# Optimization experiments

Measured on AMD Instinct MI355X. Metric: run time of the kernel, lower is better.

## Reference

```python
import jax, jax.numpy as jnp
import numpy as np

L, T, F = 16, 1 << 19, 2
N_MIN, N_MAX = 16, 2048
N_POINTS = 1 << 21
_PRIMES = (np.uint32(1), np.uint32(2654435761))


def _resolutions(L, N_min, N_max):
    if L == 1:
        return [N_min]
    b = (N_max / N_min) ** (1.0 / (L - 1))
    return [int(round(N_min * b ** l)) for l in range(L)]


def _hash(cx, cy, table_size):
    # XOR of coord_i * prime_i, mod T. T is a power of two, so uint32
    # wraparound matches torch's int64 arithmetic in the low bits.
    h = cx.astype(jnp.uint32) * _PRIMES[0]
    h = h ^ (cy.astype(jnp.uint32) * _PRIMES[1])
    return (h % jnp.uint32(table_size)).astype(jnp.int32)


def setup_inputs() -> dict:
    key = jax.random.key(0)
    k1, k2 = jax.random.split(key)
    xy = jax.random.uniform(k1, (N_POINTS, 2), dtype=jnp.float32)
    # matches torch.empty(T,F).uniform_(-1e-4, 1e-4) per level
    tables = (jax.random.uniform(k2, (L, T, F), dtype=jnp.float32) * 2.0 - 1.0) * 1e-4
    return {"xy": xy, "tables": tables}


def reference(xy, tables):
    # xy: (P, 2) in [0,1]; tables: (L, T, F). Returns (P, L*F).
    res = _resolutions(L, N_MIN, N_MAX)
    feats = []
    for l in range(L):
        N = res[l]
        scaled = xy * N                      # (P, 2)
        i0 = jnp.floor(scaled).astype(jnp.int32)
        t = scaled - i0.astype(xy.dtype)
        wx, wy = t[..., 0:1], t[..., 1:2]    # (P, 1)
        corners = []
        for dy in (0, 1):
            for dx in (0, 1):
                cx = (i0[..., 0] + dx) % N
                cy = (i0[..., 1] + dy) % N
                h = _hash(cx, cy, T)         # (P,)
                corners.append(tables[l][h]) # (P, F)
        c00, c10, c01, c11 = corners
        f0 = c00 * (1 - wx) + c10 * wx
        f1 = c01 * (1 - wx) + c11 * wx
        feats.append(f0 * (1 - wy) + f1 * wy)
    return jnp.concatenate(feats, axis=-1)   # (P, L*F)
```

## Files before the change

### kernel.cpp

```cpp
#include <hip/hip_runtime.h>
#include <math.h>

#define NPOINTS (1 << 21)
#define LVL 16
#define TSIZE (1 << 19)
#define TMASK (TSIZE - 1)
#define PRIME2 2654435761u

#define GBITS 9
#define GRES (1 << GBITS)
#define SCAN_CHUNK 1024
#define CB 1024
#define PPB 8192
#define NB1 (NPOINTS / PPB)
#define MSIZE (CB * NB1)
#define NCHUNKS (MSIZE / SCAN_CHUNK)
#define CAP 2560

typedef float f32x2 __attribute__((ext_vector_type(2)));
typedef float f32x4 __attribute__((ext_vector_type(4)));

struct Params {
    int   n[LVL];
    float fn[LVL];
};

__device__ __forceinline__ unsigned part1by1(unsigned v) {
    v &= 0xFFFFu;
    v = (v | (v << 8)) & 0x00FF00FFu;
    v = (v | (v << 4)) & 0x0F0F0F0Fu;
    v = (v | (v << 2)) & 0x33333333u;
    v = (v | (v << 1)) & 0x55555555u;
    return v;
}

__device__ __forceinline__ unsigned morton_key(f32x2 pt) {
    int kx = (int)(pt.x * (float)GRES);
    int ky = (int)(pt.y * (float)GRES);
    kx = min(max(kx, 0), GRES - 1);
    ky = min(max(ky, 0), GRES - 1);
    return (part1by1((unsigned)ky) << 1) | part1by1((unsigned)kx);
}

__device__ __forceinline__ f32x2 level_feat(const f32x2* __restrict__ tables,
                                            int l, int N, float fN, f32x2 pt)
{
    float sx = pt.x * fN;
    float sy = pt.y * fN;
    float fx = floorf(sx);
    float fy = floorf(sy);
    float wx = sx - fx;
    float wy = sy - fy;
    int ix = (int)fx;
    int iy = (int)fy;

    int cx0 = (ix     >= N) ? ix - N     : ix;
    int cx1 = (ix + 1 >= N) ? ix + 1 - N : ix + 1;
    int cy0 = (iy     >= N) ? iy - N     : iy;
    int cy1 = (iy + 1 >= N) ? iy + 1 - N : iy + 1;

    unsigned hy0 = (unsigned)cy0 * PRIME2;
    unsigned hy1 = (unsigned)cy1 * PRIME2;

    const f32x2* tbl = tables + (size_t)l * TSIZE;
    f32x2 c00 = tbl[(int)(((unsigned)cx0 ^ hy0) & TMASK)];
    f32x2 c10 = tbl[(int)(((unsigned)cx1 ^ hy0) & TMASK)];
    f32x2 c01 = tbl[(int)(((unsigned)cx0 ^ hy1) & TMASK)];
    f32x2 c11 = tbl[(int)(((unsigned)cx1 ^ hy1) & TMASK)];

    float omx = 1.0f - wx, omy = 1.0f - wy;
    float f0x = c00.x * omx + c10.x * wx;
    float f0y = c00.y * omx + c10.y * wx;
    float f1x = c01.x * omx + c11.x * wx;
    float f1y = c01.y * omx + c11.y * wx;

    f32x2 r;
    r.x = f0x * omy + f1x * wy;
    r.y = f0y * omy + f1y * wy;
    return r;
}

__global__ __launch_bounds__(256) void hist1_kernel(
    const f32x2* __restrict__ xy, unsigned* __restrict__ M)
{
    __shared__ unsigned lh[CB];
    int tid = threadIdx.x, b = blockIdx.x;
    for (int k = tid; k < CB; k += 256) lh[k] = 0;
    __syncthreads();
    int base = b * PPB;
    #pragma unroll
    for (int i = 0; i < PPB / 256; ++i) {
        f32x2 pt = __builtin_nontemporal_load(&xy[base + i * 256 + tid]);
        atomicAdd(&lh[morton_key(pt) >> 8], 1u);
    }
    __syncthreads();
    for (int k = tid; k < CB; k += 256) M[k * NB1 + b] = lh[k];
}

__global__ __launch_bounds__(SCAN_CHUNK) void scan_local_kernel(
    unsigned* __restrict__ hist, unsigned* __restrict__ aux)
{
    __shared__ unsigned s[SCAN_CHUNK];
    int t = threadIdx.x;
    int i = blockIdx.x * SCAN_CHUNK + t;
    unsigned v = hist[i];
    s[t] = v;
    __syncthreads();
    #pragma unroll
    for (int o = 1; o < SCAN_CHUNK; o <<= 1) {
        unsigned x = (t >= o) ? s[t - o] : 0u;
        __syncthreads();
        s[t] += x;
        __syncthreads();
    }
    hist[i] = s[t] - v;
    if (t == SCAN_CHUNK - 1) aux[blockIdx.x] = s[t];
}

__global__ __launch_bounds__(NCHUNKS) void scan_aux_kernel(unsigned* __restrict__ aux)
{
    __shared__ unsigned s[NCHUNKS];
    int t = threadIdx.x;
    unsigned v = aux[t];
    s[t] = v;
    __syncthreads();
    #pragma unroll
    for (int o = 1; o < NCHUNKS; o <<= 1) {
        unsigned x = (t >= o) ? s[t - o] : 0u;
        __syncthreads();
        s[t] += x;
        __syncthreads();
    }
    aux[t] = s[t] - v;
}

__global__ __launch_bounds__(256) void scatter1_kernel(
    const f32x2* __restrict__ xy, const unsigned* __restrict__ M,
    const unsigned* __restrict__ aux, f32x4* __restrict__ slotsA)
{
    __shared__ unsigned cur[CB];
    int tid = threadIdx.x, b = blockIdx.x;
    for (int k = tid; k < CB; k += 256) {
        unsigned idx = (unsigned)k * NB1 + b;
        cur[k] = M[idx] + aux[idx >> 10];
    }
    __syncthreads();
    int base = b * PPB;
    #pragma unroll
    for (int i = 0; i < PPB / 256; ++i) {
        int p = base + i * 256 + tid;
        f32x2 pt = __builtin_nontemporal_load(&xy[p]);
        unsigned k = morton_key(pt) >> 8;
        unsigned pos = atomicAdd(&cur[k], 1u);
        f32x4 s = { pt.x, pt.y, __uint_as_float((unsigned)p), 0.0f };
        slotsA[pos] = s;
    }
}

__global__ __launch_bounds__(256) void fine_kernel(
    const f32x4* __restrict__ slotsA, const unsigned* __restrict__ M,
    const unsigned* __restrict__ aux, f32x4* __restrict__ slotsB)
{
    __shared__ f32x4 buf[CAP];
    __shared__ unsigned fh[256];
    __shared__ unsigned fc[256];

    int tid = threadIdx.x;
    int k   = blockIdx.x;

    unsigned i0 = (unsigned)k * NB1;
    unsigned start = M[i0] + aux[i0 >> 10];
    unsigned end;
    if (k == CB - 1) end = NPOINTS;
    else {
        unsigned i1 = (unsigned)(k + 1) * NB1;
        end = M[i1] + aux[i1 >> 10];
    }
    unsigned n = end - start;
    unsigned m = n > CAP ? CAP : n;

    fh[tid] = 0;
    __syncthreads();
    for (unsigned i = tid; i < m; i += 256) {
        f32x4 s = slotsA[start + i];
        buf[i] = s;
        f32x2 pt = { s.x, s.y };
        atomicAdd(&fh[morton_key(pt) & 255u], 1u);
    }
    __syncthreads();
    unsigned v = fh[tid];
    fc[tid] = v;
    __syncthreads();
    #pragma unroll
    for (int o = 1; o < 256; o <<= 1) {
        unsigned x = (tid >= o) ? fc[tid - o] : 0u;
        __syncthreads();
        fc[tid] += x;
        __syncthreads();
    }
    unsigned excl = fc[tid] - v;
    __syncthreads();
    fc[tid] = excl;
    __syncthreads();
    for (unsigned i = tid; i < m; i += 256) {
        f32x4 s = buf[i];
        f32x2 pt = { s.x, s.y };
        unsigned r = atomicAdd(&fc[morton_key(pt) & 255u], 1u);
        slotsB[start + r] = s;
    }
    for (unsigned i = CAP + tid; i < n; i += 256)
        slotsB[start + i] = slotsA[start + i];
}

__global__ __launch_bounds__(256) void main_kernel(
    const f32x4* __restrict__ slots,
    const f32x2* __restrict__ tables,
    f32x4* __restrict__ out,
    Params P)
{
    int sp = blockIdx.x * 256 + threadIdx.x;
    f32x4 s = __builtin_nontemporal_load(&slots[sp]);
    f32x2 pt = { s.x, s.y };
    unsigned op = __float_as_uint(s.z);
    f32x4* o = out + (size_t)op * 8;

    f32x2 r[8];
    #pragma unroll
    for (int j = 0; j < 8; ++j)
        r[j] = level_feat(tables, j, P.n[j], P.fn[j], pt);
    #pragma unroll
    for (int q = 0; q < 4; ++q) {
        f32x4 v = { r[2 * q].x, r[2 * q].y, r[2 * q + 1].x, r[2 * q + 1].y };
        o[q] = v;
    }
    #pragma unroll
    for (int j = 0; j < 8; ++j)
        r[j] = level_feat(tables, 8 + j, P.n[8 + j], P.fn[8 + j], pt);
    #pragma unroll
    for (int q = 0; q < 4; ++q) {
        f32x4 v = { r[2 * q].x, r[2 * q].y, r[2 * q + 1].x, r[2 * q + 1].y };
        o[4 + q] = v;
    }
}

__global__ __launch_bounds__(256, 6) void hashgrid2d_fallback(
    const f32x2* __restrict__ xy,
    const f32x2* __restrict__ tables,
    f32x4* __restrict__ out,
    Params P)
{
    __shared__ f32x4 lds[256 * 5];

    int tid = threadIdx.x;
    int p   = blockIdx.x * 256 + tid;

    f32x2 pt = __builtin_nontemporal_load(&xy[p]);
    size_t base = (size_t)blockIdx.x * 2048;

    #pragma unroll
    for (int b = 0; b < 2; ++b) {
        #pragma unroll
        for (int q = 0; q < 4; ++q) {
            float f[4];
            #pragma unroll
            for (int j = 0; j < 2; ++j) {
                int l = b * 8 + q * 2 + j;
                f32x2 r = level_feat(tables, l, P.n[l], P.fn[l], pt);
                f[j * 2 + 0] = r.x;
                f[j * 2 + 1] = r.y;
            }
            f32x4 v = { f[0], f[1], f[2], f[3] };
            lds[tid * 5 + q] = v;
        }
        __syncthreads();
        #pragma unroll
        for (int i = 0; i < 4; ++i) {
            int e  = i * 256 + tid;
            int pp = e >> 2;
            int q  = e & 3;
            f32x4 v = lds[pp * 5 + q];
            __builtin_nontemporal_store(v, &out[base + pp * 8 + b * 4 + q]);
        }
        __syncthreads();
    }
}

extern "C" void kernel_launch(void* const* d_in, const int* in_sizes, int n_in,
                              void* d_out, int out_size, void* d_ws, size_t ws_size,
                              hipStream_t stream) {
    const f32x2* xy     = (const f32x2*)d_in[0];
    const f32x2* tables = (const f32x2*)d_in[1];
    f32x4* out = (f32x4*)d_out;

    Params P;
    double b = pow(2048.0 / 16.0, 1.0 / 15.0);
    for (int l = 0; l < LVL; ++l) {
        int N = (int)llround(16.0 * pow(b, (double)l));
        P.n[l]  = N;
        P.fn[l] = (float)N;
    }

    const size_t WS_NEED = 66u << 20;

    if (ws_size >= WS_NEED) {
        char* w = (char*)d_ws;
        unsigned* M      = (unsigned*)(w);
        unsigned* aux    = (unsigned*)(w + (1u << 20));
        f32x4*    slotsA = (f32x4*)   (w + (2u << 20));
        f32x4*    slotsB = (f32x4*)   (w + (34u << 20));

        hist1_kernel     <<<NB1,           256,        0, stream>>>(xy, M);
        scan_local_kernel<<<NCHUNKS,       SCAN_CHUNK, 0, stream>>>(M, aux);
        scan_aux_kernel  <<<1,             NCHUNKS,    0, stream>>>(aux);
        scatter1_kernel  <<<NB1,           256,        0, stream>>>(xy, M, aux, slotsA);
        fine_kernel      <<<CB,            256,        0, stream>>>(slotsA, M, aux, slotsB);
        main_kernel      <<<NPOINTS / 256, 256,        0, stream>>>(slotsB, tables, out, P);
    } else {
        hashgrid2d_fallback<<<NPOINTS / 256, 256, 0, stream>>>(xy, tables, out, P);
    }
}
```

Measured before the change: 266.7 us.

## Process two Morton-adjacent points per thread and share corner loads per level

Each main_kernel thread now handles two consecutive sorted points and, per level, skips the four table gathers for the second point when it falls in the same grid cell as the first. Block indices are also remapped with an XCD-style swizzle so that neighbouring slot ranges are spread differently across the chip. The aim is fewer redundant gathers at coarse levels, where adjacent points usually share a cell. In exchange the kernel uses more registers and introduces a divergent branch, and each thread's slot loads are now strided, which weakens coalescing.

```diff
diff --git a/kernel.cpp b/kernel.cpp
--- a/kernel.cpp
+++ b/kernel.cpp
@@ -80,6 +80,69 @@
     return r;
 }
 
+__device__ __forceinline__ void level_pair(
+    const f32x2* __restrict__ tables, int l, int N, float fN,
+    f32x2 pa, f32x2 pb, f32x2& ra, f32x2& rb)
+{
+    const f32x2* tbl = tables + (size_t)l * TSIZE;
+
+    float sxa = pa.x * fN, sya = pa.y * fN;
+    float fxa = floorf(sxa), fya = floorf(sya);
+    float wxa = sxa - fxa, wya = sya - fya;
+    int ixa = (int)fxa, iya = (int)fya;
+
+    int cx0a = (ixa     >= N) ? ixa - N     : ixa;
+    int cx1a = (ixa + 1 >= N) ? ixa + 1 - N : ixa + 1;
+    int cy0a = (iya     >= N) ? iya - N     : iya;
+    int cy1a = (iya + 1 >= N) ? iya + 1 - N : iya + 1;
+
+    unsigned hy0a = (unsigned)cy0a * PRIME2;
+    unsigned hy1a = (unsigned)cy1a * PRIME2;
+    f32x2 c00 = tbl[(int)(((unsigned)cx0a ^ hy0a) & TMASK)];
+    f32x2 c10 = tbl[(int)(((unsigned)cx1a ^ hy0a) & TMASK)];
+    f32x2 c01 = tbl[(int)(((unsigned)cx0a ^ hy1a) & TMASK)];
+    f32x2 c11 = tbl[(int)(((unsigned)cx1a ^ hy1a) & TMASK)];
+
+    {
+        float omx = 1.0f - wxa, omy = 1.0f - wya;
+        float f0x = c00.x * omx + c10.x * wxa;
+        float f0y = c00.y * omx + c10.y * wxa;
+        float f1x = c01.x * omx + c11.x * wxa;
+        float f1y = c01.y * omx + c11.y * wxa;
+        ra.x = f0x * omy + f1x * wya;
+        ra.y = f0y * omy + f1y * wya;
+    }
+
+    float sxb = pb.x * fN, syb = pb.y * fN;
+    float fxb = floorf(sxb), fyb = floorf(syb);
+    float wxb = sxb - fxb, wyb = syb - fyb;
+    int ixb = (int)fxb, iyb = (int)fyb;
+
+    f32x2 d00 = c00, d10 = c10, d01 = c01, d11 = c11;
+    if (!(ixb == ixa && iyb == iya)) {
+        int cx0b = (ixb     >= N) ? ixb - N     : ixb;
+        int cx1b = (ixb + 1 >= N) ? ixb + 1 - N : ixb + 1;
+        int cy0b = (iyb     >= N) ? iyb - N     : iyb;
+        int cy1b = (iyb + 1 >= N) ? iyb + 1 - N : iyb + 1;
+        unsigned hy0b = (unsigned)cy0b * PRIME2;
+        unsigned hy1b = (unsigned)cy1b * PRIME2;
+        d00 = tbl[(int)(((unsigned)cx0b ^ hy0b) & TMASK)];
+        d10 = tbl[(int)(((unsigned)cx1b ^ hy0b) & TMASK)];
+        d01 = tbl[(int)(((unsigned)cx0b ^ hy1b) & TMASK)];
+        d11 = tbl[(int)(((unsigned)cx1b ^ hy1b) & TMASK)];
+    }
+
+    {
+        float omx = 1.0f - wxb, omy = 1.0f - wyb;
+        float f0x = d00.x * omx + d10.x * wxb;
+        float f0y = d00.y * omx + d10.y * wxb;
+        float f1x = d01.x * omx + d11.x * wxb;
+        float f1y = d01.y * omx + d11.y * wxb;
+        rb.x = f0x * omy + f1x * wyb;
+        rb.y = f0y * omy + f1y * wyb;
+    }
+}
+
 __global__ __launch_bounds__(256) void hist1_kernel(
     const f32x2* __restrict__ xy, unsigned* __restrict__ M)
 {
@@ -218,28 +281,32 @@
     f32x4* __restrict__ out,
     Params P)
 {
-    int sp = blockIdx.x * 256 + threadIdx.x;
-    f32x4 s = __builtin_nontemporal_load(&slots[sp]);
-    f32x2 pt = { s.x, s.y };
-    unsigned op = __float_as_uint(s.z);
-    f32x4* o = out + (size_t)op * 8;
-
-    f32x2 r[8];
-    #pragma unroll
-    for (int j = 0; j < 8; ++j)
-        r[j] = level_feat(tables, j, P.n[j], P.fn[j], pt);
-    #pragma unroll
-    for (int q = 0; q < 4; ++q) {
-        f32x4 v = { r[2 * q].x, r[2 * q].y, r[2 * q + 1].x, r[2 * q + 1].y };
-        o[q] = v;
-    }
-    #pragma unroll
-    for (int j = 0; j < 8; ++j)
-        r[j] = level_feat(tables, 8 + j, P.n[8 + j], P.fn[8 + j], pt);
-    #pragma unroll
-    for (int q = 0; q < 4; ++q) {
-        f32x4 v = { r[2 * q].x, r[2 * q].y, r[2 * q + 1].x, r[2 * q + 1].y };
-        o[4 + q] = v;
+    int bid = (blockIdx.x & 7) * 512 + (blockIdx.x >> 3);
+    int t   = bid * 256 + threadIdx.x;
+    int sp0 = t * 2;
+
+    f32x4 s0 = __builtin_nontemporal_load(&slots[sp0]);
+    f32x4 s1 = __builtin_nontemporal_load(&slots[sp0 + 1]);
+    f32x2 pa = { s0.x, s0.y };
+    f32x2 pb = { s1.x, s1.y };
+    unsigned opa = __float_as_uint(s0.z);
+    unsigned opb = __float_as_uint(s1.z);
+    f32x4* oa = out + (size_t)opa * 8;
+    f32x4* ob = out + (size_t)opb * 8;
+
+    #pragma unroll
+    for (int hb = 0; hb < 2; ++hb) {
+        #pragma unroll
+        for (int q = 0; q < 4; ++q) {
+            int l = hb * 8 + q * 2;
+            f32x2 ra0, rb0, ra1, rb1;
+            level_pair(tables, l,     P.n[l],     P.fn[l],     pa, pb, ra0, rb0);
+            level_pair(tables, l + 1, P.n[l + 1], P.fn[l + 1], pa, pb, ra1, rb1);
+            f32x4 va = { ra0.x, ra0.y, ra1.x, ra1.y };
+            f32x4 vb = { rb0.x, rb0.y, rb1.x, rb1.y };
+            oa[hb * 4 + q] = va;
+            ob[hb * 4 + q] = vb;
+        }
     }
 }
 
@@ -314,7 +381,7 @@
         scan_aux_kernel  <<<1,             NCHUNKS,    0, stream>>>(aux);
         scatter1_kernel  <<<NB1,           256,        0, stream>>>(xy, M, aux, slotsA);
         fine_kernel      <<<CB,            256,        0, stream>>>(slotsA, M, aux, slotsB);
-        main_kernel      <<<NPOINTS / 256, 256,        0, stream>>>(slotsB, tables, out, P);
+        main_kernel      <<<NPOINTS / 512, 256,        0, stream>>>(slotsB, tables, out, P);
     } else {
         hashgrid2d_fallback<<<NPOINTS / 256, 256, 0, stream>>>(xy, tables, out, P);
     }
```

After: 335.8 us. +25.9%, slower.
